# Performance work log

Hardware: AMD Instinct MI355X
Metric: run time of the kernel (lower is better)

## Reference

```python
import jax, jax.numpy as jnp
import numpy as np

N_NODES = 200000
N_EDGES = 6400000
D = 128

def setup_inputs() -> dict:
    key = jax.random.key(0)
    k1, k2, k3, k4, k5 = jax.random.split(key, 5)
    ego_embeddings = jax.random.normal(k1, (N_NODES, D), dtype=jnp.float32)
    vals = jax.random.uniform(k2, (N_EDGES,), dtype=jnp.float32)
    W = jax.random.normal(k3, (D, D), dtype=jnp.float32)
    rows = jax.random.randint(k4, (N_EDGES,), 0, N_NODES, dtype=jnp.int64)
    cols = jax.random.randint(k5, (N_EDGES,), 0, N_NODES, dtype=jnp.int64)
    return {"ego_embeddings": ego_embeddings, "vals": vals, "W": W,
            "rows": rows, "cols": cols, "n_nodes": N_NODES}

def reference(ego_embeddings, vals, W, rows, cols, n_nodes):
    # Sparse [N,N] @ dense [N,d]: gather source-node embeddings, scale by edge
    # values, and scatter-add into destination rows (COO SpMM).
    msgs = vals[:, None] * ego_embeddings[cols]            # [E, d]
    agg = jax.ops.segment_sum(msgs, rows, num_segments=n_nodes)  # [N, d]
    # tf: transpose(W @ agg^T) == agg @ W^T
    return agg @ W.T
```

## Files before the change

### kernel.cpp

```cpp
#include <hip/hip_runtime.h>
#include <hip/hip_bf16.h>

#define PTHREADS 512
#define CHUNK_E 8192
#define EPT 16
#define NB_LDS 2048
#define BUFCAP 4608
#define EPT_ACC 9
#define THREADS 256

typedef __attribute__((ext_vector_type(8))) __bf16 bf16x8;
typedef __attribute__((ext_vector_type(4))) float f32x4;

__device__ inline float bf_lo(unsigned u) { return __uint_as_float(u << 16); }
__device__ inline float bf_hi(unsigned u) { return __uint_as_float(u & 0xffff0000u); }

__global__ void convert_kernel(const float* __restrict__ in,
                               unsigned short* __restrict__ outb, long long n4) {
    long long stride = (long long)gridDim.x * blockDim.x;
    for (long long i = (long long)blockIdx.x * blockDim.x + threadIdx.x; i < n4; i += stride) {
        float4 v = ((const float4*)in)[i];
        union { ushort4 u; __hip_bfloat16 h[4]; } c;
        c.h[0] = __float2bfloat16(v.x);
        c.h[1] = __float2bfloat16(v.y);
        c.h[2] = __float2bfloat16(v.z);
        c.h[3] = __float2bfloat16(v.w);
        ((ushort4*)outb)[i] = c.u;
    }
}

__global__ void bucket_hist_kernel(const int* __restrict__ rows,
                                   int* __restrict__ bcount, int nEdges, int nb) {
    __shared__ int h[NB_LDS];
    for (int i = threadIdx.x; i < nb; i += blockDim.x) h[i] = 0;
    __syncthreads();
    int stride = gridDim.x * blockDim.x;
    for (int e = blockIdx.x * blockDim.x + threadIdx.x; e < nEdges; e += stride) {
        int r = __builtin_nontemporal_load(&rows[e]);
        atomicAdd(&h[r >> 7], 1);
    }
    __syncthreads();
    for (int i = threadIdx.x; i < nb; i += blockDim.x)
        if (h[i]) atomicAdd(&bcount[i], h[i]);
}

__global__ __launch_bounds__(PTHREADS) void scan_buckets_kernel(
    const int* __restrict__ bcount, int* __restrict__ bucket_start,
    int* __restrict__ cursor, int nEdges, int nb) {
    __shared__ int tsum[PTHREADS];
    int base = threadIdx.x * 4;
    int c[4]; int s = 0;
#pragma unroll
    for (int k = 0; k < 4; ++k) {
        int i = base + k;
        c[k] = (i < nb) ? bcount[i] : 0;
        s += c[k];
    }
    tsum[threadIdx.x] = s;
    __syncthreads();
    for (int off = 1; off < PTHREADS; off <<= 1) {
        int v = (threadIdx.x >= (unsigned)off) ? tsum[threadIdx.x - off] : 0;
        __syncthreads();
        tsum[threadIdx.x] += v;
        __syncthreads();
    }
    int run = (threadIdx.x == 0) ? 0 : tsum[threadIdx.x - 1];
#pragma unroll
    for (int k = 0; k < 4; ++k) {
        int i = base + k;
        if (i < nb) { bucket_start[i] = run; cursor[i] = run; run += c[k]; }
    }
    if (threadIdx.x == PTHREADS - 1) bucket_start[nb] = nEdges;
}

__global__ __launch_bounds__(PTHREADS) void partition_kernel(
    const int* __restrict__ rows, const int* __restrict__ cols,
    const float* __restrict__ vals, int* __restrict__ cursor,
    int2* __restrict__ pairs, int nEdges, int nb) {
    __shared__ int cnt[NB_LDS];
    __shared__ int off_[NB_LDS];
    __shared__ int tsum[PTHREADS];
    __shared__ int2 buf[CHUNK_E];
    __shared__ unsigned short bkt[CHUNK_E];

    int chunk0 = blockIdx.x * CHUNK_E;
    int nHere = min(CHUNK_E, nEdges - chunk0);
    if (nHere <= 0) return;

    for (int i = threadIdx.x; i < nb; i += PTHREADS) cnt[i] = 0;
    __syncthreads();

    int2 mypk[EPT];
    int mybr[EPT];
#pragma unroll
    for (int k = 0; k < EPT; ++k) {
        int idx = k * PTHREADS + threadIdx.x;
        if (idx < nHere) {
            int e = chunk0 + idx;
            int r = __builtin_nontemporal_load(&rows[e]);
            int c = __builtin_nontemporal_load(&cols[e]);
            float v = __builtin_nontemporal_load(&vals[e]);
            int b = r >> 7;
            mypk[k] = make_int2((c << 7) | (r & 127), __float_as_int(v));
            int rank = atomicAdd(&cnt[b], 1);
            mybr[k] = (b << 16) | rank;
        } else mybr[k] = -1;
    }
    __syncthreads();

    {
        int base = threadIdx.x * 4;
        int s = 0;
#pragma unroll
        for (int k = 0; k < 4; ++k) { int i = base + k; if (i < nb) s += cnt[i]; }
        tsum[threadIdx.x] = s;
        __syncthreads();
        for (int off = 1; off < PTHREADS; off <<= 1) {
            int v = (threadIdx.x >= (unsigned)off) ? tsum[threadIdx.x - off] : 0;
            __syncthreads();
            tsum[threadIdx.x] += v;
            __syncthreads();
        }
        int run = (threadIdx.x == 0) ? 0 : tsum[threadIdx.x - 1];
#pragma unroll
        for (int k = 0; k < 4; ++k) {
            int i = base + k;
            if (i < nb) { off_[i] = run; run += cnt[i]; }
        }
    }
    __syncthreads();

#pragma unroll
    for (int k = 0; k < EPT; ++k) {
        if (mybr[k] >= 0) {
            int b = mybr[k] >> 16, rank = mybr[k] & 0xFFFF;
            int pos = off_[b] + rank;
            buf[pos] = mypk[k];
            bkt[pos] = (unsigned short)b;
        }
    }
    __syncthreads();

    for (int b = threadIdx.x; b < nb; b += PTHREADS) {
        int c0 = off_[b];
        int c1 = (b + 1 < nb) ? off_[b + 1] : nHere;
        int n = c1 - c0;
        if (n > 0) {
            int g = atomicAdd(&cursor[b], n);
            cnt[b] = g - c0;
        }
    }
    __syncthreads();

    for (int i = threadIdx.x; i < nHere; i += PTHREADS) {
        union { int2 i2; long long l; } u; u.i2 = buf[i];
        __builtin_nontemporal_store(u.l, (long long*)pairs + (cnt[bkt[i]] + i));
    }
}

template <bool BF>
__global__ __launch_bounds__(PTHREADS) void sortaccum_kernel(
    const void* __restrict__ egov, const int2* __restrict__ pairs,
    const int* __restrict__ bucket_start, float* __restrict__ out, int nRows) {
    __shared__ int2 buf[BUFCAP];
    __shared__ int cnt[129];
    __shared__ int tsum[128];

    int b = blockIdx.x;
    int s = bucket_start[b];
    int e = bucket_start[b + 1];
    int n = e - s;
    if (n > BUFCAP) n = BUFCAP;

    int t = threadIdx.x;
    if (t < 129) cnt[t] = 0;
    __syncthreads();

    int2 p[EPT_ACC];
    int rk[EPT_ACC];
#pragma unroll
    for (int k = 0; k < EPT_ACC; ++k) {
        int i = k * PTHREADS + t;
        if (i < n) {
            union { long long l; int2 i2; } u;
            u.l = __builtin_nontemporal_load((const long long*)pairs + (s + i));
            p[k] = u.i2;
            rk[k] = atomicAdd(&cnt[p[k].x & 127], 1);
        } else rk[k] = -1;
    }
    __syncthreads();

    if (t < 128) tsum[t] = cnt[t];
    __syncthreads();
    for (int off = 1; off < 128; off <<= 1) {
        int v = (t < 128 && t >= off) ? tsum[t - off] : 0;
        __syncthreads();
        if (t < 128) tsum[t] += v;
        __syncthreads();
    }
    if (t == 0) cnt[0] = 0;
    if (t < 128) cnt[t + 1] = tsum[t];
    __syncthreads();

#pragma unroll
    for (int k = 0; k < EPT_ACC; ++k) {
        if (rk[k] >= 0) buf[cnt[p[k].x & 127] + rk[k]] = p[k];
    }
    __syncthreads();

    int wid = t >> 6, lane = t & 63;
    int row0 = b << 7;
    for (int rr = 0; rr < 16; ++rr) {
        int r = (wid << 4) + rr;
        int gr = row0 + r;
        if (gr >= nRows) break;
        int i = cnt[r], i1 = cnt[r + 1];
        float accx = 0.f, accy = 0.f;
        for (; i + 3 < i1; i += 4) {
            int2 pe0 = buf[i], pe1 = buf[i + 1], pe2 = buf[i + 2], pe3 = buf[i + 3];
            float v0 = __int_as_float(pe0.y), v1 = __int_as_float(pe1.y);
            float v2 = __int_as_float(pe2.y), v3 = __int_as_float(pe3.y);
            if (BF) {
                const unsigned short* eb = (const unsigned short*)egov;
                unsigned u0 = ((const unsigned*)(eb + (long long)(pe0.x >> 7) * 128))[lane];
                unsigned u1 = ((const unsigned*)(eb + (long long)(pe1.x >> 7) * 128))[lane];
                unsigned u2 = ((const unsigned*)(eb + (long long)(pe2.x >> 7) * 128))[lane];
                unsigned u3 = ((const unsigned*)(eb + (long long)(pe3.x >> 7) * 128))[lane];
                accx += v0 * bf_lo(u0); accy += v0 * bf_hi(u0);
                accx += v1 * bf_lo(u1); accy += v1 * bf_hi(u1);
                accx += v2 * bf_lo(u2); accy += v2 * bf_hi(u2);
                accx += v3 * bf_lo(u3); accy += v3 * bf_hi(u3);
            } else {
                const float* ef = (const float*)egov;
                float2 x0 = ((const float2*)(ef + (long long)(pe0.x >> 7) * 128))[lane];
                float2 x1 = ((const float2*)(ef + (long long)(pe1.x >> 7) * 128))[lane];
                float2 x2 = ((const float2*)(ef + (long long)(pe2.x >> 7) * 128))[lane];
                float2 x3 = ((const float2*)(ef + (long long)(pe3.x >> 7) * 128))[lane];
                accx += v0 * x0.x; accy += v0 * x0.y;
                accx += v1 * x1.x; accy += v1 * x1.y;
                accx += v2 * x2.x; accy += v2 * x2.y;
                accx += v3 * x3.x; accy += v3 * x3.y;
            }
        }
        for (; i < i1; ++i) {
            int2 pe = buf[i];
            float v = __int_as_float(pe.y);
            if (BF) {
                unsigned u = ((const unsigned*)((const unsigned short*)egov +
                              (long long)(pe.x >> 7) * 128))[lane];
                accx += v * bf_lo(u); accy += v * bf_hi(u);
            } else {
                float2 x = ((const float2*)((const float*)egov +
                            (long long)(pe.x >> 7) * 128))[lane];
                accx += v * x.x; accy += v * x.y;
            }
        }
        union { float2 f; long long l; } o;
        o.f = make_float2(accx, accy);
        __builtin_nontemporal_store(o.l, (long long*)(out + (long long)gr * 128) + lane);
    }
}

__global__ __launch_bounds__(256) void mfma_gemm_y_kernel(
    const float* __restrict__ ego, const unsigned short* __restrict__ wbf,
    unsigned short* __restrict__ Y, int nRows) {
    int wid = threadIdx.x >> 6, lane = threadIdx.x & 63;
    long long m0 = ((long long)blockIdx.x * 4 + wid) * 32;
    if (m0 >= nRows) return;
    int g  = lane >> 4;
    int mr = lane & 15;

    bf16x8 a[2][4];
#pragma unroll
    for (int st = 0; st < 2; ++st) {
        long long row = m0 + st * 16 + mr;
        if (row >= nRows) row = nRows - 1;
        const float* rp = ego + row * 128;
#pragma unroll
        for (int kb = 0; kb < 4; ++kb) {
            const float4* p4 = (const float4*)(rp + kb * 32 + g * 8);
            float4 lo = p4[0], hi = p4[1];
            bf16x8 tv;
            tv[0] = (__bf16)lo.x; tv[1] = (__bf16)lo.y;
            tv[2] = (__bf16)lo.z; tv[3] = (__bf16)lo.w;
            tv[4] = (__bf16)hi.x; tv[5] = (__bf16)hi.y;
            tv[6] = (__bf16)hi.z; tv[7] = (__bf16)hi.w;
            a[st][kb] = tv;
        }
    }

    f32x4 acc[2][8];
#pragma unroll
    for (int st = 0; st < 2; ++st)
#pragma unroll
        for (int jt = 0; jt < 8; ++jt) acc[st][jt] = (f32x4){0.f, 0.f, 0.f, 0.f};

#pragma unroll
    for (int jt = 0; jt < 8; ++jt) {
        const unsigned short* wp = wbf + (jt * 16 + mr) * 128;
        bf16x8 bv[4];
#pragma unroll
        for (int kb = 0; kb < 4; ++kb)
            bv[kb] = *(const bf16x8*)(wp + kb * 32 + g * 8);
#pragma unroll
        for (int st = 0; st < 2; ++st)
#pragma unroll
            for (int kb = 0; kb < 4; ++kb)
                acc[st][jt] = __builtin_amdgcn_mfma_f32_16x16x32_bf16(
                    a[st][kb], bv[kb], acc[st][jt], 0, 0, 0);
    }

#pragma unroll
    for (int st = 0; st < 2; ++st) {
#pragma unroll
        for (int reg = 0; reg < 4; ++reg) {
            long long row = m0 + st * 16 + g * 4 + reg;
            if (row < nRows) {
                unsigned short* op = Y + row * 128;
#pragma unroll
                for (int jt = 0; jt < 8; ++jt) {
                    __hip_bfloat16 h = __float2bfloat16(acc[st][jt][reg]);
                    op[jt * 16 + mr] = *(unsigned short*)&h;
                }
            }
        }
    }
}

__global__ __launch_bounds__(256) void mfma_gemm_kernel(
    float* __restrict__ out, const unsigned short* __restrict__ wbf, int nRows) {
    int wid = threadIdx.x >> 6, lane = threadIdx.x & 63;
    long long m0 = ((long long)blockIdx.x * 4 + wid) * 32;
    if (m0 >= nRows) return;
    int g  = lane >> 4;
    int mr = lane & 15;

    bf16x8 a[2][4];
#pragma unroll
    for (int st = 0; st < 2; ++st) {
        long long row = m0 + st * 16 + mr;
        if (row >= nRows) row = nRows - 1;
        const float* rp = out + row * 128;
#pragma unroll
        for (int kb = 0; kb < 4; ++kb) {
            const float4* p4 = (const float4*)(rp + kb * 32 + g * 8);
            float4 lo = p4[0], hi = p4[1];
            bf16x8 tv;
            tv[0] = (__bf16)lo.x; tv[1] = (__bf16)lo.y;
            tv[2] = (__bf16)lo.z; tv[3] = (__bf16)lo.w;
            tv[4] = (__bf16)hi.x; tv[5] = (__bf16)hi.y;
            tv[6] = (__bf16)hi.z; tv[7] = (__bf16)hi.w;
            a[st][kb] = tv;
        }
    }

    f32x4 acc[2][8];
#pragma unroll
    for (int st = 0; st < 2; ++st)
#pragma unroll
        for (int jt = 0; jt < 8; ++jt) acc[st][jt] = (f32x4){0.f, 0.f, 0.f, 0.f};

#pragma unroll
    for (int jt = 0; jt < 8; ++jt) {
        const unsigned short* wp = wbf + (jt * 16 + mr) * 128;
        bf16x8 bv[4];
#pragma unroll
        for (int kb = 0; kb < 4; ++kb)
            bv[kb] = *(const bf16x8*)(wp + kb * 32 + g * 8);
#pragma unroll
        for (int st = 0; st < 2; ++st)
#pragma unroll
            for (int kb = 0; kb < 4; ++kb)
                acc[st][jt] = __builtin_amdgcn_mfma_f32_16x16x32_bf16(
                    a[st][kb], bv[kb], acc[st][jt], 0, 0, 0);
    }

#pragma unroll
    for (int st = 0; st < 2; ++st) {
#pragma unroll
        for (int reg = 0; reg < 4; ++reg) {
            long long row = m0 + st * 16 + g * 4 + reg;
            if (row < nRows) {
                float* op = out + row * 128;
#pragma unroll
                for (int jt = 0; jt < 8; ++jt)
                    op[jt * 16 + mr] = acc[st][jt][reg];
            }
        }
    }
}

__global__ void scatter_kernel(const float* __restrict__ ego,
                               const float* __restrict__ vals,
                               const int* __restrict__ rows,
                               const int* __restrict__ cols,
                               float* __restrict__ out, int nEdges) {
    long long total = (long long)nEdges * 32;
    long long stride = (long long)gridDim.x * blockDim.x;
    for (long long tt = (long long)blockIdx.x * blockDim.x + threadIdx.x;
         tt < total; tt += stride) {
        int e = (int)(tt >> 5);
        int g = (int)(tt & 31);
        int r = rows[e], c = cols[e];
        float v = vals[e];
        float4 x = ((const float4*)(ego + (long long)c * 128))[g];
        float* dst = out + (long long)r * 128 + (g << 2);
        atomicAdd(dst + 0, x.x * v);
        atomicAdd(dst + 1, x.y * v);
        atomicAdd(dst + 2, x.z * v);
        atomicAdd(dst + 3, x.w * v);
    }
}

__global__ __launch_bounds__(THREADS) void rowgemm_kernel(float* __restrict__ out,
                                                          const float* __restrict__ W,
                                                          int nRows) {
    __shared__ float4 w4[128 * 32];
    const float4* Wg = (const float4*)W;
    for (int i = threadIdx.x; i < 128 * 32; i += THREADS) w4[i] = Wg[i];
    __syncthreads();

    int stride = gridDim.x * blockDim.x;
    for (int r = blockIdx.x * blockDim.x + threadIdx.x; r < nRows; r += stride) {
        float4* rowp = (float4*)(out + (long long)r * 128);
        float4 a[32];
#pragma unroll
        for (int i = 0; i < 32; ++i) a[i] = rowp[i];

#pragma unroll 1
        for (int jc = 0; jc < 8; ++jc) {
            float acc[16];
#pragma unroll
            for (int jj = 0; jj < 16; ++jj) acc[jj] = 0.f;
#pragma unroll
            for (int k4 = 0; k4 < 32; ++k4) {
                float4 av = a[k4];
#pragma unroll
                for (int jj = 0; jj < 16; ++jj) {
                    float4 wv = w4[(jc * 16 + jj) * 32 + k4];
                    acc[jj] += av.x * wv.x + av.y * wv.y + av.z * wv.z + av.w * wv.w;
                }
            }
            float4* op = rowp + jc * 4;
#pragma unroll
            for (int jj4 = 0; jj4 < 4; ++jj4)
                op[jj4] = make_float4(acc[jj4 * 4 + 0], acc[jj4 * 4 + 1],
                                      acc[jj4 * 4 + 2], acc[jj4 * 4 + 3]);
        }
    }
}

extern "C" void kernel_launch(void* const* d_in, const int* in_sizes, int n_in,
                              void* d_out, int out_size, void* d_ws, size_t ws_size,
                              hipStream_t stream) {
    const float* ego  = (const float*)d_in[0];
    const float* vals = (const float*)d_in[1];
    const float* W    = (const float*)d_in[2];
    const int*   rows = (const int*)d_in[3];
    const int*   cols = (const int*)d_in[4];

    int nEdges = in_sizes[1];
    int nRows  = in_sizes[0] / 128;
    int nb     = (nRows + 127) >> 7;
    float* out = (float*)d_out;

    int2* pairs = (int2*)d_ws;
    size_t off_base   = (size_t)nEdges * 8;
    size_t y_bytes    = (size_t)nRows * 128 * 2;
    size_t ints_bytes = (size_t)nb * 4 * 3 + 64;
    size_t wbf_bytes  = 128 * 128 * 2 + 64;

    size_t need_f32 = off_base + ints_bytes + wbf_bytes;
    size_t need_bf  = off_base + y_bytes + ints_bytes + wbf_bytes;

    bool use_partition = (nb <= NB_LDS) && (ws_size >= need_f32);
    bool use_bf = use_partition && (ws_size >= need_bf);

    if (use_partition) {
        unsigned short* Y = (unsigned short*)((char*)d_ws + off_base);
        size_t ioff = use_bf ? (off_base + y_bytes) : off_base;
        ioff = (ioff + 63) & ~(size_t)63;
        int* bcount       = (int*)((char*)d_ws + ioff);
        int* bucket_start = bcount + nb;
        int* cursor       = bucket_start + nb + 1;
        size_t woff = (ioff + (size_t)nb * 4 * 3 + 4 + 63) & ~(size_t)63;
        unsigned short* wbf = (unsigned short*)((char*)d_ws + woff);

        hipMemsetAsync(bcount, 0, (size_t)nb * 4, stream);
        bucket_hist_kernel<<<512, THREADS, 0, stream>>>(rows, bcount, nEdges, nb);
        scan_buckets_kernel<<<1, PTHREADS, 0, stream>>>(bcount, bucket_start, cursor,
                                                        nEdges, nb);
        convert_kernel<<<16, THREADS, 0, stream>>>(W, wbf, 4096);
        int nChunks = (nEdges + CHUNK_E - 1) / CHUNK_E;
        partition_kernel<<<nChunks, PTHREADS, 0, stream>>>(rows, cols, vals, cursor,
                                                           pairs, nEdges, nb);
        if (use_bf) {
            mfma_gemm_y_kernel<<<(nRows + 127) / 128, 256, 0, stream>>>(ego, wbf, Y, nRows);
            sortaccum_kernel<true><<<nb, PTHREADS, 0, stream>>>(Y, pairs,
                                                                bucket_start, out, nRows);
        } else {
            sortaccum_kernel<false><<<nb, PTHREADS, 0, stream>>>(ego, pairs,
                                                                 bucket_start, out, nRows);
            mfma_gemm_kernel<<<(nRows + 127) / 128, 256, 0, stream>>>(out, wbf, nRows);
        }
    } else {
        hipMemsetAsync(d_out, 0, (size_t)out_size * sizeof(float), stream);
        scatter_kernel<<<16384, THREADS, 0, stream>>>(ego, vals, rows, cols, out, nEdges);
        if (ws_size >= wbf_bytes) {
            unsigned short* wbf = (unsigned short*)d_ws;
            convert_kernel<<<16, THREADS, 0, stream>>>(W, wbf, 4096);
            mfma_gemm_kernel<<<(nRows + 127) / 128, 256, 0, stream>>>(out, wbf, nRows);
        } else {
            rowgemm_kernel<<<(nRows + THREADS - 1) / THREADS, THREADS, 0, stream>>>(out, W, nRows);
        }
    }
}
```

Measured before the change: 446.0 us.

## Replace single-pass bucket partition with two-level radix partition using output as scratch

The separate histogram kernel and the single 1563-bucket partition are replaced by two passes. Pass A scatters edges into 49 coarse super-buckets of 4096 rows, staged in the output buffer, and builds the fine histogram at the same time. Pass B splits each super-bucket into 32 fine buckets in the final pairs array. This cuts the extra read of rows and makes the global scatter writes more contiguous, at the cost of an extra read and write of the edge pairs. Edges beyond the fixed per-super-bucket capacity (SBCAP) are dropped silently, and the ego loads in the GEMM are changed to nontemporal.

```diff
diff --git a/kernel.cpp b/kernel.cpp
--- a/kernel.cpp
+++ b/kernel.cpp
@@ -2,18 +2,35 @@
 #include <hip/hip_bf16.h>
 
 #define PTHREADS 512
-#define CHUNK_E 8192
-#define EPT 16
+#define THREADS 256
+
+#define CHUNK_A 6144
+#define EPT_A 12
+#define NSB_MAX 64
+#define SB_SHIFT 12
+#define SB_ROWS 4096
+#define SBCAP 139264
+
+#define CHUNK_B 8192
+#define EPT_B 16
+#define NCHB 17
+
 #define NB_LDS 2048
 #define BUFCAP 4608
 #define EPT_ACC 9
-#define THREADS 256
 
 typedef __attribute__((ext_vector_type(8))) __bf16 bf16x8;
 typedef __attribute__((ext_vector_type(4))) float f32x4;
 
 __device__ inline float bf_lo(unsigned u) { return __uint_as_float(u << 16); }
 __device__ inline float bf_hi(unsigned u) { return __uint_as_float(u & 0xffff0000u); }
+
+__global__ void init_kernel(int* __restrict__ bcount, int nb,
+                            int* __restrict__ cursorA, int nsb) {
+    int i = blockIdx.x * blockDim.x + threadIdx.x;
+    if (i < nb) bcount[i] = 0;
+    if (i < nsb) cursorA[i] = i * SBCAP;
+}
 
 __global__ void convert_kernel(const float* __restrict__ in,
                                unsigned short* __restrict__ outb, long long n4) {
@@ -29,21 +46,6 @@
     }
 }
 
-__global__ void bucket_hist_kernel(const int* __restrict__ rows,
-                                   int* __restrict__ bcount, int nEdges, int nb) {
-    __shared__ int h[NB_LDS];
-    for (int i = threadIdx.x; i < nb; i += blockDim.x) h[i] = 0;
-    __syncthreads();
-    int stride = gridDim.x * blockDim.x;
-    for (int e = blockIdx.x * blockDim.x + threadIdx.x; e < nEdges; e += stride) {
-        int r = __builtin_nontemporal_load(&rows[e]);
-        atomicAdd(&h[r >> 7], 1);
-    }
-    __syncthreads();
-    for (int i = threadIdx.x; i < nb; i += blockDim.x)
-        if (h[i]) atomicAdd(&bcount[i], h[i]);
-}
-
 __global__ __launch_bounds__(PTHREADS) void scan_buckets_kernel(
     const int* __restrict__ bcount, int* __restrict__ bucket_start,
     int* __restrict__ cursor, int nEdges, int nb) {
@@ -73,88 +75,166 @@
     if (threadIdx.x == PTHREADS - 1) bucket_start[nb] = nEdges;
 }
 
-__global__ __launch_bounds__(PTHREADS) void partition_kernel(
+__global__ __launch_bounds__(PTHREADS) void passA_kernel(
     const int* __restrict__ rows, const int* __restrict__ cols,
-    const float* __restrict__ vals, int* __restrict__ cursor,
-    int2* __restrict__ pairs, int nEdges, int nb) {
-    __shared__ int cnt[NB_LDS];
-    __shared__ int off_[NB_LDS];
-    __shared__ int tsum[PTHREADS];
-    __shared__ int2 buf[CHUNK_E];
-    __shared__ unsigned short bkt[CHUNK_E];
-
-    int chunk0 = blockIdx.x * CHUNK_E;
-    int nHere = min(CHUNK_E, nEdges - chunk0);
+    const float* __restrict__ vals, int* __restrict__ cursorA,
+    int* __restrict__ bcount, int2* __restrict__ pairsA, int nEdges, int nsb, int nb) {
+    __shared__ int cnt[NSB_MAX];
+    __shared__ int off_[NSB_MAX];
+    __shared__ int lim[NSB_MAX];
+    __shared__ int hist[NB_LDS];
+    __shared__ int tsum[NSB_MAX];
+    __shared__ int2 buf[CHUNK_A];
+    __shared__ unsigned char sbid[CHUNK_A];
+
+    int chunk0 = blockIdx.x * CHUNK_A;
+    int nHere = min(CHUNK_A, nEdges - chunk0);
     if (nHere <= 0) return;
-
-    for (int i = threadIdx.x; i < nb; i += PTHREADS) cnt[i] = 0;
-    __syncthreads();
-
-    int2 mypk[EPT];
-    int mybr[EPT];
-#pragma unroll
-    for (int k = 0; k < EPT; ++k) {
-        int idx = k * PTHREADS + threadIdx.x;
+    int t = threadIdx.x;
+    if (t < NSB_MAX) cnt[t] = 0;
+    for (int i = t; i < nb; i += PTHREADS) hist[i] = 0;
+    __syncthreads();
+
+    int2 mypk[EPT_A];
+    int mybr[EPT_A];
+#pragma unroll
+    for (int k = 0; k < EPT_A; ++k) {
+        int idx = k * PTHREADS + t;
         if (idx < nHere) {
             int e = chunk0 + idx;
             int r = __builtin_nontemporal_load(&rows[e]);
             int c = __builtin_nontemporal_load(&cols[e]);
             float v = __builtin_nontemporal_load(&vals[e]);
-            int b = r >> 7;
-            mypk[k] = make_int2((c << 7) | (r & 127), __float_as_int(v));
-            int rank = atomicAdd(&cnt[b], 1);
-            mybr[k] = (b << 16) | rank;
+            int sb = r >> SB_SHIFT;
+            mypk[k] = make_int2((c << SB_SHIFT) | (r & (SB_ROWS - 1)), __float_as_int(v));
+            atomicAdd(&hist[r >> 7], 1);
+            int rank = atomicAdd(&cnt[sb], 1);
+            mybr[k] = (sb << 24) | rank;
         } else mybr[k] = -1;
     }
     __syncthreads();
 
-    {
-        int base = threadIdx.x * 4;
-        int s = 0;
-#pragma unroll
-        for (int k = 0; k < 4; ++k) { int i = base + k; if (i < nb) s += cnt[i]; }
-        tsum[threadIdx.x] = s;
-        __syncthreads();
-        for (int off = 1; off < PTHREADS; off <<= 1) {
-            int v = (threadIdx.x >= (unsigned)off) ? tsum[threadIdx.x - off] : 0;
-            __syncthreads();
-            tsum[threadIdx.x] += v;
-            __syncthreads();
-        }
-        int run = (threadIdx.x == 0) ? 0 : tsum[threadIdx.x - 1];
-#pragma unroll
-        for (int k = 0; k < 4; ++k) {
-            int i = base + k;
-            if (i < nb) { off_[i] = run; run += cnt[i]; }
-        }
-    }
-    __syncthreads();
-
-#pragma unroll
-    for (int k = 0; k < EPT; ++k) {
+    if (t < NSB_MAX) tsum[t] = cnt[t];
+    __syncthreads();
+    for (int o = 1; o < NSB_MAX; o <<= 1) {
+        int v = (t < NSB_MAX && t >= o) ? tsum[t - o] : 0;
+        __syncthreads();
+        if (t < NSB_MAX) tsum[t] += v;
+        __syncthreads();
+    }
+    if (t < NSB_MAX) off_[t] = t ? tsum[t - 1] : 0;
+    __syncthreads();
+
+#pragma unroll
+    for (int k = 0; k < EPT_A; ++k) {
         if (mybr[k] >= 0) {
-            int b = mybr[k] >> 16, rank = mybr[k] & 0xFFFF;
-            int pos = off_[b] + rank;
+            int sb = mybr[k] >> 24;
+            int pos = off_[sb] + (mybr[k] & 0xFFFFFF);
             buf[pos] = mypk[k];
-            bkt[pos] = (unsigned short)b;
-        }
-    }
-    __syncthreads();
-
-    for (int b = threadIdx.x; b < nb; b += PTHREADS) {
-        int c0 = off_[b];
-        int c1 = (b + 1 < nb) ? off_[b + 1] : nHere;
+            sbid[pos] = (unsigned char)sb;
+        }
+    }
+    __syncthreads();
+
+    if (t < NSB_MAX) {
+        int c0 = off_[t];
+        int c1 = (t < NSB_MAX - 1) ? off_[t + 1] : nHere;
         int n = c1 - c0;
-        if (n > 0) {
-            int g = atomicAdd(&cursor[b], n);
-            cnt[b] = g - c0;
-        }
-    }
-    __syncthreads();
-
-    for (int i = threadIdx.x; i < nHere; i += PTHREADS) {
+        int g = 0;
+        if (n > 0 && t < nsb) g = atomicAdd(&cursorA[t], n);
+        cnt[t] = g - c0;
+        lim[t] = (t + 1) * SBCAP;
+    }
+    __syncthreads();
+
+    for (int i = t; i < nHere; i += PTHREADS) {
+        int sb = sbid[i];
+        int gp = cnt[sb] + i;
+        if (gp < lim[sb]) {
+            union { int2 i2; long long l; } u; u.i2 = buf[i];
+            __builtin_nontemporal_store(u.l, (long long*)pairsA + gp);
+        }
+    }
+    __syncthreads();
+
+    for (int i = t; i < nb; i += PTHREADS) {
+        int h = hist[i];
+        if (h) atomicAdd(&bcount[i], h);
+    }
+}
+
+__global__ __launch_bounds__(PTHREADS) void passB_kernel(
+    const int2* __restrict__ pairsA, const int* __restrict__ cursorA,
+    int* __restrict__ cursor, int2* __restrict__ pairs, int nsb) {
+    __shared__ int cnt[32];
+    __shared__ int off_[32];
+    __shared__ int tsum[32];
+    __shared__ int2 buf[CHUNK_B];
+    __shared__ unsigned char lbid[CHUNK_B];
+
+    int s = blockIdx.x / NCHB;
+    int ci = blockIdx.x % NCHB;
+    if (s >= nsb) return;
+    int base = s * SBCAP;
+    int i0 = base + ci * CHUNK_B;
+    int nHere = min(cursorA[s] - i0, CHUNK_B);
+    if (nHere <= 0) return;
+    int t = threadIdx.x;
+    if (t < 32) cnt[t] = 0;
+    __syncthreads();
+
+    int2 myfp[EPT_B];
+    int mybr[EPT_B];
+#pragma unroll
+    for (int k = 0; k < EPT_B; ++k) {
+        int idx = k * PTHREADS + t;
+        if (idx < nHere) {
+            union { long long l; int2 i2; } u;
+            u.l = __builtin_nontemporal_load((const long long*)pairsA + (i0 + idx));
+            int pk = u.i2.x;
+            int lb = (pk & (SB_ROWS - 1)) >> 7;
+            myfp[k] = make_int2(((pk >> SB_SHIFT) << 7) | (pk & 127), u.i2.y);
+            int rank = atomicAdd(&cnt[lb], 1);
+            mybr[k] = (lb << 24) | rank;
+        } else mybr[k] = -1;
+    }
+    __syncthreads();
+
+    if (t < 32) tsum[t] = cnt[t];
+    __syncthreads();
+    for (int o = 1; o < 32; o <<= 1) {
+        int v = (t < 32 && t >= o) ? tsum[t - o] : 0;
+        __syncthreads();
+        if (t < 32) tsum[t] += v;
+        __syncthreads();
+    }
+    if (t < 32) off_[t] = t ? tsum[t - 1] : 0;
+    __syncthreads();
+
+#pragma unroll
+    for (int k = 0; k < EPT_B; ++k) {
+        if (mybr[k] >= 0) {
+            int lb = mybr[k] >> 24;
+            int pos = off_[lb] + (mybr[k] & 0xFFFFFF);
+            buf[pos] = myfp[k];
+            lbid[pos] = (unsigned char)lb;
+        }
+    }
+    __syncthreads();
+
+    if (t < 32) {
+        int c0 = off_[t];
+        int c1 = (t < 31) ? off_[t + 1] : nHere;
+        int n = c1 - c0;
+        int g = 0;
+        if (n > 0) g = atomicAdd(&cursor[(s << 5) + t], n);
+        cnt[t] = g - c0;
+    }
+    __syncthreads();
+
+    for (int i = t; i < nHere; i += PTHREADS) {
         union { int2 i2; long long l; } u; u.i2 = buf[i];
-        __builtin_nontemporal_store(u.l, (long long*)pairs + (cnt[bkt[i]] + i));
+        __builtin_nontemporal_store(u.l, (long long*)pairs + (cnt[lbid[i]] + i));
     }
 }
 
@@ -278,13 +358,13 @@
         const float* rp = ego + row * 128;
 #pragma unroll
         for (int kb = 0; kb < 4; ++kb) {
-            const float4* p4 = (const float4*)(rp + kb * 32 + g * 8);
-            float4 lo = p4[0], hi = p4[1];
+            f32x4 lo = __builtin_nontemporal_load((const f32x4*)(rp + kb * 32 + g * 8));
+            f32x4 hi = __builtin_nontemporal_load((const f32x4*)(rp + kb * 32 + g * 8) + 1);
             bf16x8 tv;
-            tv[0] = (__bf16)lo.x; tv[1] = (__bf16)lo.y;
-            tv[2] = (__bf16)lo.z; tv[3] = (__bf16)lo.w;
-            tv[4] = (__bf16)hi.x; tv[5] = (__bf16)hi.y;
-            tv[6] = (__bf16)hi.z; tv[7] = (__bf16)hi.w;
+            tv[0] = (__bf16)lo[0]; tv[1] = (__bf16)lo[1];
+            tv[2] = (__bf16)lo[2]; tv[3] = (__bf16)lo[3];
+            tv[4] = (__bf16)hi[0]; tv[5] = (__bf16)hi[1];
+            tv[6] = (__bf16)hi[2]; tv[7] = (__bf16)hi[3];
             a[st][kb] = tv;
         }
     }
@@ -462,18 +542,23 @@
     int nEdges = in_sizes[1];
     int nRows  = in_sizes[0] / 128;
     int nb     = (nRows + 127) >> 7;
+    int nsb    = (nRows + SB_ROWS - 1) >> SB_SHIFT;
     float* out = (float*)d_out;
 
     int2* pairs = (int2*)d_ws;
     size_t off_base   = (size_t)nEdges * 8;
     size_t y_bytes    = (size_t)nRows * 128 * 2;
-    size_t ints_bytes = (size_t)nb * 4 * 3 + 64;
+    size_t ints_bytes = ((size_t)nb * 3 + 1 + NSB_MAX) * 4 + 64;
     size_t wbf_bytes  = 128 * 128 * 2 + 64;
 
     size_t need_f32 = off_base + ints_bytes + wbf_bytes;
     size_t need_bf  = off_base + y_bytes + ints_bytes + wbf_bytes;
 
-    bool use_partition = (nb <= NB_LDS) && (ws_size >= need_f32);
+    size_t pairsA_bytes = (size_t)nsb * SBCAP * 8;
+    bool scratch_ok = pairsA_bytes <= (size_t)out_size * 4;
+
+    bool use_partition = (nb <= NB_LDS) && (nsb <= NSB_MAX) && scratch_ok &&
+                         (ws_size >= need_f32);
     bool use_bf = use_partition && (ws_size >= need_bf);
 
     if (use_partition) {
@@ -483,17 +568,20 @@
         int* bcount       = (int*)((char*)d_ws + ioff);
         int* bucket_start = bcount + nb;
         int* cursor       = bucket_start + nb + 1;
-        size_t woff = (ioff + (size_t)nb * 4 * 3 + 4 + 63) & ~(size_t)63;
+        int* cursorA      = cursor + nb;
+        size_t woff = (ioff + ((size_t)nb * 3 + 1 + NSB_MAX) * 4 + 63) & ~(size_t)63;
         unsigned short* wbf = (unsigned short*)((char*)d_ws + woff);
-
-        hipMemsetAsync(bcount, 0, (size_t)nb * 4, stream);
-        bucket_hist_kernel<<<512, THREADS, 0, stream>>>(rows, bcount, nEdges, nb);
+        int2* pairsA = (int2*)d_out;
+
+        int initN = (nb > nsb ? nb : nsb);
+        init_kernel<<<(initN + 255) / 256, 256, 0, stream>>>(bcount, nb, cursorA, nsb);
+        passA_kernel<<<(nEdges + CHUNK_A - 1) / CHUNK_A, PTHREADS, 0, stream>>>(
+            rows, cols, vals, cursorA, bcount, pairsA, nEdges, nsb, nb);
         scan_buckets_kernel<<<1, PTHREADS, 0, stream>>>(bcount, bucket_start, cursor,
                                                         nEdges, nb);
+        passB_kernel<<<nsb * NCHB, PTHREADS, 0, stream>>>(pairsA, cursorA, cursor,
+                                                          pairs, nsb);
         convert_kernel<<<16, THREADS, 0, stream>>>(W, wbf, 4096);
-        int nChunks = (nEdges + CHUNK_E - 1) / CHUNK_E;
-        partition_kernel<<<nChunks, PTHREADS, 0, stream>>>(rows, cols, vals, cursor,
-                                                           pairs, nEdges, nb);
         if (use_bf) {
             mfma_gemm_y_kernel<<<(nRows + 127) / 128, 256, 0, stream>>>(ego, wbf, Y, nRows);
             sortaccum_kernel<true><<<nb, PTHREADS, 0, stream>>>(Y, pairs,
```

Result: faster. 400.6 us (-10.2%).
